# Performance work log

Hardware: AMD Instinct MI355X
Metric: run time of the kernel (lower is better)

The kernel has to match this reference:

```python
import jax, jax.numpy as jnp
import numpy as np

VOCAB = 32000
EMBED = 2048
RANK = 16
N_ADAPTERS = 8
S = 16384


def setup_inputs() -> dict:
    key = jax.random.key(0)
    k1, k2, k3, k4, k5 = jax.random.split(key, 5)
    input_ids = jax.random.randint(k1, (S,), 0, VOCAB, dtype=jnp.int64 if jax.config.jax_enable_x64 else jnp.int32)
    adapter_ids = jax.random.randint(k2, (S,), 0, N_ADAPTERS, dtype=input_ids.dtype)
    weight = jax.random.normal(k3, (VOCAB, EMBED), dtype=jnp.float32)
    embedding_A = jax.random.normal(k4, (N_ADAPTERS, VOCAB, RANK), dtype=jnp.float32)
    embedding_B = jax.random.normal(k5, (N_ADAPTERS, EMBED, RANK), dtype=jnp.float32)
    return {"input_ids": input_ids, "adapter_ids": adapter_ids, "weight": weight,
            "embedding_A": embedding_A, "embedding_B": embedding_B}


def reference(input_ids, adapter_ids, weight, embedding_A, embedding_B):
    # mask out-of-vocab (extra) tokens to id 0 for the base gather
    added_mask = input_ids > (VOCAB - 1)
    masked_ids = jnp.where(added_mask, 0, input_ids)
    # base embedding lookup: [S, EMBED]
    base_output = weight[masked_ids]
    # per-token adapter-routed LoRA-A embedding gather: [S, RANK]
    lora_a_out = embedding_A[adapter_ids, masked_ids]
    # grouped LoRA-B sgemm: per-token B[adapter] @ a, fused with base add
    # B[adapter_ids]: [S, EMBED, RANK]
    out = base_output + jnp.einsum('sr,ser->se', lora_a_out, embedding_B[adapter_ids])
    return out
```

## Files before the change

kernel.cpp:

```cpp
#include <hip/hip_runtime.h>

#define VOCAB   32000
#define EMBED   2048
#define RANK    16
#define NADAPT  8
#define S_TOK   16384
#define T_TOK   128
#define GRP     8
#define ECHUNK  256

__global__ __launch_bounds__(256, 2)
void lora_embed_kernel(const int* __restrict__ input_ids,
                       const int* __restrict__ adapter_ids,
                       const float* __restrict__ weight,
                       const float* __restrict__ embA,
                       const float* __restrict__ embB,
                       float* __restrict__ out)
{
    const int tid    = threadIdx.x;
    const int echunk = blockIdx.x & 7;
    const int tchunk = blockIdx.x >> 3;
    const int e      = echunk * ECHUNK + tid;
    const int t0     = tchunk * T_TOK;

    __shared__ int   ids_s[T_TOK];
    __shared__ int   ads_s[T_TOK];
    __shared__ float a_s[T_TOK][RANK];

    if (tid < T_TOK) {
        int id = input_ids[t0 + tid];
        if (id > VOCAB - 1) id = 0;
        ids_s[tid] = id;
        ads_s[tid] = adapter_ids[t0 + tid];
    }
    __syncthreads();

    for (int j = tid; j < T_TOK * RANK; j += 256) {
        const int i = j >> 4, r = j & 15;
        a_s[i][r] = embA[((long)ads_s[i] * VOCAB + ids_s[i]) * RANK + r];
    }

    float4 b[NADAPT][4];
    const float4* B4 = (const float4*)embB;
    #pragma unroll
    for (int ad = 0; ad < NADAPT; ++ad) {
        #pragma unroll
        for (int c = 0; c < 4; ++c)
            b[ad][c] = B4[((long)ad * EMBED + e) * 4 + c];
    }
    __syncthreads();

    for (int g = 0; g < T_TOK; g += GRP) {
        float basev[GRP];
        int   adg[GRP];
        #pragma unroll
        for (int u = 0; u < GRP; ++u) {
            const int id = __builtin_amdgcn_readfirstlane(ids_s[g + u]);
            adg[u]       = __builtin_amdgcn_readfirstlane(ads_s[g + u]);
            basev[u] = weight[(long)id * EMBED + e];
        }
        #pragma unroll
        for (int u = 0; u < GRP; ++u) {
            const int i = g + u;
            const float4 a0 = *(const float4*)&a_s[i][0];
            const float4 a1 = *(const float4*)&a_s[i][4];
            const float4 a2 = *(const float4*)&a_s[i][8];
            const float4 a3 = *(const float4*)&a_s[i][12];
            float acc = basev[u];
            switch (adg[u]) {
#define CASE(K) case K: \
                acc += a0.x*b[K][0].x + a0.y*b[K][0].y + a0.z*b[K][0].z + a0.w*b[K][0].w \
                     + a1.x*b[K][1].x + a1.y*b[K][1].y + a1.z*b[K][1].z + a1.w*b[K][1].w \
                     + a2.x*b[K][2].x + a2.y*b[K][2].y + a2.z*b[K][2].z + a2.w*b[K][2].w \
                     + a3.x*b[K][3].x + a3.y*b[K][3].y + a3.z*b[K][3].z + a3.w*b[K][3].w; \
                break;
                CASE(0) CASE(1) CASE(2) CASE(3) CASE(4) CASE(5) CASE(6) CASE(7)
#undef CASE
            }
            out[(long)(t0 + i) * EMBED + e] = acc;
        }
    }
}

extern "C" void kernel_launch(void* const* d_in, const int* in_sizes, int n_in,
                              void* d_out, int out_size, void* d_ws, size_t ws_size,
                              hipStream_t stream) {
    const int*   input_ids   = (const int*)d_in[0];
    const int*   adapter_ids = (const int*)d_in[1];
    const float* weight      = (const float*)d_in[2];
    const float* embA        = (const float*)d_in[3];
    const float* embB        = (const float*)d_in[4];
    float*       out         = (float*)d_out;

    dim3 grid((S_TOK / T_TOK) * (EMBED / ECHUNK));
    dim3 block(256);
    hipLaunchKernelGGL(lora_embed_kernel, grid, block, 0, stream,
                       input_ids, adapter_ids, weight, embA, embB, out);
}
```

Before: 404.8 us.

## Bucket tokens by adapter so each block uses a single LoRA-B slice

Adds a pre-pass kernel that groups token indices by adapter id via shared and global atomics, packing the vocab id and token index into one int. The main kernel then processes one adapter per block, loading only that adapter's B row into registers and dropping the 8-way switch. This cuts register pressure, so occupancy is raised to 4 waves and the token tile is doubled. The cost is an extra memset and kernel launch, scattered output writes, and many blocks that exit early. The packing assumes vocab ids and token indices each fit in 16 bits, and token order within a bucket depends on atomic ordering.

```diff
diff --git a/kernel.cpp b/kernel.cpp
--- a/kernel.cpp
+++ b/kernel.cpp
@@ -5,13 +5,37 @@
 #define RANK    16
 #define NADAPT  8
 #define S_TOK   16384
-#define T_TOK   128
+#define T_TOK   256
 #define GRP     8
 #define ECHUNK  256
 
-__global__ __launch_bounds__(256, 2)
-void lora_embed_kernel(const int* __restrict__ input_ids,
-                       const int* __restrict__ adapter_ids,
+__global__ __launch_bounds__(256)
+void bucket_kernel(const int* __restrict__ input_ids,
+                   const int* __restrict__ adapter_ids,
+                   int* __restrict__ counters,
+                   int* __restrict__ bucket)
+{
+    const int tid = threadIdx.x;
+    const int t   = blockIdx.x * 256 + tid;
+    int id = input_ids[t];
+    if (id > VOCAB - 1) id = 0;
+    const int ad = adapter_ids[t];
+
+    __shared__ int hist[NADAPT];
+    __shared__ int base[NADAPT];
+    if (tid < NADAPT) hist[tid] = 0;
+    __syncthreads();
+    const int rank = atomicAdd(&hist[ad], 1);
+    __syncthreads();
+    if (tid < NADAPT)
+        base[tid] = atomicAdd(&counters[tid], hist[tid]);
+    __syncthreads();
+    bucket[ad * S_TOK + base[ad] + rank] = (id << 16) | t;
+}
+
+__global__ __launch_bounds__(256, 4)
+void lora_embed_kernel(const int* __restrict__ counters,
+                       const int* __restrict__ bucket,
                        const float* __restrict__ weight,
                        const float* __restrict__ embA,
                        const float* __restrict__ embB,
@@ -19,44 +43,40 @@
 {
     const int tid    = threadIdx.x;
     const int echunk = blockIdx.x & 7;
-    const int tchunk = blockIdx.x >> 3;
-    const int e      = echunk * ECHUNK + tid;
-    const int t0     = tchunk * T_TOK;
+    const int chunk  = (blockIdx.x >> 3) & 63;
+    const int ad     = blockIdx.x >> 9;
 
-    __shared__ int   ids_s[T_TOK];
-    __shared__ int   ads_s[T_TOK];
+    const int n     = counters[ad];
+    const int start = chunk * T_TOK;
+    if (start >= n) return;
+    const int cnt = min(T_TOK, n - start);
+    const int e   = echunk * ECHUNK + tid;
+
+    __shared__ int   pk_s[T_TOK];
     __shared__ float a_s[T_TOK][RANK];
 
-    if (tid < T_TOK) {
-        int id = input_ids[t0 + tid];
-        if (id > VOCAB - 1) id = 0;
-        ids_s[tid] = id;
-        ads_s[tid] = adapter_ids[t0 + tid];
-    }
+    if (tid < cnt) pk_s[tid] = bucket[ad * S_TOK + start + tid];
     __syncthreads();
 
-    for (int j = tid; j < T_TOK * RANK; j += 256) {
+    for (int j = tid; j < cnt * RANK; j += 256) {
         const int i = j >> 4, r = j & 15;
-        a_s[i][r] = embA[((long)ads_s[i] * VOCAB + ids_s[i]) * RANK + r];
+        const int id = ((unsigned)pk_s[i]) >> 16;
+        a_s[i][r] = embA[((long)ad * VOCAB + id) * RANK + r];
     }
 
-    float4 b[NADAPT][4];
-    const float4* B4 = (const float4*)embB;
-    #pragma unroll
-    for (int ad = 0; ad < NADAPT; ++ad) {
-        #pragma unroll
-        for (int c = 0; c < 4; ++c)
-            b[ad][c] = B4[((long)ad * EMBED + e) * 4 + c];
-    }
+    const float4* B4 = (const float4*)embB + ((long)ad * EMBED + e) * 4;
+    const float4 b0 = B4[0], b1 = B4[1], b2 = B4[2], b3 = B4[3];
     __syncthreads();
 
-    for (int g = 0; g < T_TOK; g += GRP) {
+    int g = 0;
+    for (; g + GRP <= cnt; g += GRP) {
         float basev[GRP];
-        int   adg[GRP];
+        int   idxg[GRP];
         #pragma unroll
         for (int u = 0; u < GRP; ++u) {
-            const int id = __builtin_amdgcn_readfirstlane(ids_s[g + u]);
-            adg[u]       = __builtin_amdgcn_readfirstlane(ads_s[g + u]);
+            const int pk = __builtin_amdgcn_readfirstlane(pk_s[g + u]);
+            idxg[u] = pk & 0xFFFF;
+            const int id = ((unsigned)pk) >> 16;
             basev[u] = weight[(long)id * EMBED + e];
         }
         #pragma unroll
@@ -67,18 +87,35 @@
             const float4 a2 = *(const float4*)&a_s[i][8];
             const float4 a3 = *(const float4*)&a_s[i][12];
             float acc = basev[u];
-            switch (adg[u]) {
-#define CASE(K) case K: \
-                acc += a0.x*b[K][0].x + a0.y*b[K][0].y + a0.z*b[K][0].z + a0.w*b[K][0].w \
-                     + a1.x*b[K][1].x + a1.y*b[K][1].y + a1.z*b[K][1].z + a1.w*b[K][1].w \
-                     + a2.x*b[K][2].x + a2.y*b[K][2].y + a2.z*b[K][2].z + a2.w*b[K][2].w \
-                     + a3.x*b[K][3].x + a3.y*b[K][3].y + a3.z*b[K][3].z + a3.w*b[K][3].w; \
-                break;
-                CASE(0) CASE(1) CASE(2) CASE(3) CASE(4) CASE(5) CASE(6) CASE(7)
-#undef CASE
-            }
-            out[(long)(t0 + i) * EMBED + e] = acc;
+            acc = fmaf(a0.x, b0.x, acc); acc = fmaf(a0.y, b0.y, acc);
+            acc = fmaf(a0.z, b0.z, acc); acc = fmaf(a0.w, b0.w, acc);
+            acc = fmaf(a1.x, b1.x, acc); acc = fmaf(a1.y, b1.y, acc);
+            acc = fmaf(a1.z, b1.z, acc); acc = fmaf(a1.w, b1.w, acc);
+            acc = fmaf(a2.x, b2.x, acc); acc = fmaf(a2.y, b2.y, acc);
+            acc = fmaf(a2.z, b2.z, acc); acc = fmaf(a2.w, b2.w, acc);
+            acc = fmaf(a3.x, b3.x, acc); acc = fmaf(a3.y, b3.y, acc);
+            acc = fmaf(a3.z, b3.z, acc); acc = fmaf(a3.w, b3.w, acc);
+            out[(long)idxg[u] * EMBED + e] = acc;
         }
+    }
+    for (; g < cnt; ++g) {
+        const int pk = __builtin_amdgcn_readfirstlane(pk_s[g]);
+        const int idx = pk & 0xFFFF;
+        const int id  = ((unsigned)pk) >> 16;
+        float acc = weight[(long)id * EMBED + e];
+        const float4 a0 = *(const float4*)&a_s[g][0];
+        const float4 a1 = *(const float4*)&a_s[g][4];
+        const float4 a2 = *(const float4*)&a_s[g][8];
+        const float4 a3 = *(const float4*)&a_s[g][12];
+        acc = fmaf(a0.x, b0.x, acc); acc = fmaf(a0.y, b0.y, acc);
+        acc = fmaf(a0.z, b0.z, acc); acc = fmaf(a0.w, b0.w, acc);
+        acc = fmaf(a1.x, b1.x, acc); acc = fmaf(a1.y, b1.y, acc);
+        acc = fmaf(a1.z, b1.z, acc); acc = fmaf(a1.w, b1.w, acc);
+        acc = fmaf(a2.x, b2.x, acc); acc = fmaf(a2.y, b2.y, acc);
+        acc = fmaf(a2.z, b2.z, acc); acc = fmaf(a2.w, b2.w, acc);
+        acc = fmaf(a3.x, b3.x, acc); acc = fmaf(a3.y, b3.y, acc);
+        acc = fmaf(a3.z, b3.z, acc); acc = fmaf(a3.w, b3.w, acc);
+        out[(long)idx * EMBED + e] = acc;
     }
 }
 
@@ -92,8 +129,16 @@
     const float* embB        = (const float*)d_in[4];
     float*       out         = (float*)d_out;
 
-    dim3 grid((S_TOK / T_TOK) * (EMBED / ECHUNK));
-    dim3 block(256);
-    hipLaunchKernelGGL(lora_embed_kernel, grid, block, 0, stream,
-                       input_ids, adapter_ids, weight, embA, embB, out);
+    int* counters = (int*)d_ws;
+    int* bucket   = counters + NADAPT;
+
+    hipMemsetAsync(counters, 0, NADAPT * sizeof(int), stream);
+
+    hipLaunchKernelGGL(bucket_kernel, dim3(S_TOK / 256), dim3(256), 0, stream,
+                       input_ids, adapter_ids, counters, bucket);
+
+    hipLaunchKernelGGL(lora_embed_kernel,
+                       dim3(NADAPT * (S_TOK / T_TOK) * (EMBED / ECHUNK)), dim3(256),
+                       0, stream,
+                       counters, bucket, weight, embA, embB, out);
 }
```

After: 426.1 us. 5.2% more time.
